# Performance work log

Measured on AMD Instinct MI355X. Metric: run time of the kernel, lower is better.

The kernel has to match this reference:

```python
import jax, jax.numpy as jnp
import numpy as np

B, T, C = 4, 2048, 2048
H, HKV = 16, 4
D = C // H            # 128
G = H // HKV          # 4 query heads per kv head
ROPE_THETA = 10000.0


def _rope_tables(seq_len, head_dim, theta):
    inv = 1.0 / (theta ** (np.arange(0, head_dim, 2, dtype=np.float32) / head_dim))
    t = np.arange(seq_len, dtype=np.float32)
    f = np.outer(t, inv)  # (T, D/2)
    return jnp.asarray(np.cos(f)), jnp.asarray(np.sin(f))


def setup_inputs() -> dict:
    key = jax.random.key(0)
    ks = jax.random.split(key, 5)
    x = jax.random.normal(ks[0], (B, T, C), dtype=jnp.float32)
    W_q = jax.random.normal(ks[1], (H * D, C), dtype=jnp.float32) * 0.02
    W_k = jax.random.normal(ks[2], (HKV * D, C), dtype=jnp.float32) * 0.02
    W_v = jax.random.normal(ks[3], (HKV * D, C), dtype=jnp.float32) * 0.02
    W_o = jax.random.normal(ks[4], (C, C), dtype=jnp.float32) * 0.02
    cos, sin = _rope_tables(T, D, ROPE_THETA)
    return {"x": x, "W_q": W_q, "W_k": W_k, "W_v": W_v, "W_o": W_o,
            "cos": cos, "sin": sin}


def _apply_rope(xh, cos, sin):
    # xh: (B, h, T, D); cos/sin: (T, D/2)
    x0 = xh[..., 0::2]
    x1 = xh[..., 1::2]
    c = cos[None, None, :, :]
    s = sin[None, None, :, :]
    o0 = x0 * c - x1 * s
    o1 = x0 * s + x1 * c
    return jnp.stack([o0, o1], axis=-1).reshape(xh.shape)


def reference(x, W_q, W_k, W_v, W_o, cos, sin):
    b, t, c = x.shape
    q = (x @ W_q.T).reshape(b, t, H, D).transpose(0, 2, 1, 3)      # (B,H,T,D)
    k = (x @ W_k.T).reshape(b, t, HKV, D).transpose(0, 2, 1, 3)    # (B,HKV,T,D)
    v = (x @ W_v.T).reshape(b, t, HKV, D).transpose(0, 2, 1, 3)
    q = _apply_rope(q, cos[:t], sin[:t])
    k = _apply_rope(k, cos[:t], sin[:t])
    # GQA via reshape instead of repeat_interleave (same head ordering:
    # q head index h = kv*G + g).
    qg = q.reshape(b, HKV, G, t, D)
    scores = jnp.einsum('bkgtd,bksd->bkgts', qg, k) / jnp.sqrt(jnp.float32(D))
    causal = jnp.tril(jnp.ones((t, t), dtype=bool))
    scores = jnp.where(causal[None, None, None, :, :], scores, -jnp.inf)
    attn = jax.nn.softmax(scores, axis=-1)
    out = jnp.einsum('bkgts,bksd->bkgtd', attn, v)                 # (B,HKV,G,T,D)
    out = out.reshape(b, H, t, D).transpose(0, 2, 1, 3).reshape(b, t, c)
    return out @ W_o.T
```

## Files before the change

### kernel.cpp

```cpp
#include <hip/hip_runtime.h>
#include <cmath>

typedef __attribute__((ext_vector_type(8))) short bf16x8;
typedef __attribute__((ext_vector_type(4))) float f32x4;
typedef __attribute__((ext_vector_type(16))) float f32x16;
typedef unsigned short u16;

__device__ __forceinline__ u16 f2bf(float f) {
  union { float f; unsigned u; } x; x.f = f;
  return (u16)((x.u + 0x7FFFu + ((x.u >> 16) & 1u)) >> 16);
}

__device__ __forceinline__ unsigned cvtpk(float lo, float hi) {
  unsigned r;
  asm("v_cvt_pk_bf16_f32 %0, %1, %2" : "=v"(r) : "v"(lo), "v"(hi));
  return r;
}

__device__ __forceinline__ void gload_lds16(const void* g, void* l) {
  __builtin_amdgcn_global_load_lds((const __attribute__((address_space(1))) unsigned*)g,
                                   (__attribute__((address_space(3))) unsigned*)l,
                                   16, 0, 0);
}

__global__ __launch_bounds__(256) void cast_all_kernel(const float* __restrict__ x,
                                                       const float* __restrict__ wq,
                                                       const float* __restrict__ wk,
                                                       const float* __restrict__ wv,
                                                       const float* __restrict__ wo,
                                                       u16* __restrict__ out) {
  const long b1 = 16777216, b2 = 20971520, b3 = 22020096, b4 = 23068672, b5 = 27262976;
  long i = (long)blockIdx.x * blockDim.x + threadIdx.x;
  long stride = (long)gridDim.x * blockDim.x;
  for (long j = i * 4; j < b5; j += stride * 4) {
    const float* src; long off;
    if (j < b1)      { src = x;  off = j; }
    else if (j < b2) { src = wq; off = j - b1; }
    else if (j < b3) { src = wk; off = j - b2; }
    else if (j < b4) { src = wv; off = j - b3; }
    else             { src = wo; off = j - b4; }
    float4 v = *(const float4*)(src + off);
    ushort4 o;
    o.x = f2bf(v.x); o.y = f2bf(v.y); o.z = f2bf(v.z); o.w = f2bf(v.w);
    *(ushort4*)(out + j) = o;
  }
}

template <int EPI>
__global__ __launch_bounds__(512, 2) void gemm_bt256(const u16* __restrict__ A,
                                                     const u16* __restrict__ B,
                                                     void* __restrict__ outp,
                                                     int M, int N, int K,
                                                     const float* __restrict__ cosp,
                                                     const float* __restrict__ sinp,
                                                     float scale) {
  __shared__ u16 lds[65536];
  const int tid = threadIdx.x;
  const int lane = tid & 63;
  const int l16 = lane & 15, lhi = lane >> 4;
  const int w = tid >> 6;
  const int wr = w >> 2, wc = w & 3;
  const int m0 = blockIdx.y * 256;
  const int n0 = blockIdx.x * 256;

  f32x4 acc[8][4];
#pragma unroll
  for (int i = 0; i < 8; ++i)
#pragma unroll
    for (int j = 0; j < 4; ++j) acc[i][j] = (f32x4)0.0f;

  const int NT = K >> 6;

  auto stage = [&](int t, int buf) {
    const int k0 = t << 6;
    u16* Ad = lds + buf * 32768;
    u16* Bd = Ad + 16384;
#pragma unroll
    for (int j = 0; j < 4; ++j) {
      int c = tid + j * 512;
      int row = c >> 3;
      int sboff = ((c & 7) * 16) ^ ((row & 7) << 4);
      gload_lds16(A + (size_t)(m0 + row) * K + k0 + (sboff >> 1), Ad + (size_t)c * 8);
    }
#pragma unroll
    for (int j = 0; j < 4; ++j) {
      int c = tid + j * 512;
      int row = c >> 3;
      int sboff = ((c & 7) * 16) ^ ((row & 7) << 4);
      gload_lds16(B + (size_t)(n0 + row) * K + k0 + (sboff >> 1), Bd + (size_t)c * 8);
    }
  };

  stage(0, 0);
  stage(1, 1);

  for (int t = 0; t < NT; ++t) {
    const int cur = t & 1;
    if (t + 1 < NT) { asm volatile("s_waitcnt vmcnt(8)" ::: "memory"); }
    else            { asm volatile("s_waitcnt vmcnt(0)" ::: "memory"); }
    __builtin_amdgcn_s_barrier();
    const char* Ab = (const char*)(lds + cur * 32768);
    const char* Bb = (const char*)(lds + cur * 32768 + 16384);
#pragma unroll
    for (int qm = 0; qm < 2; ++qm)
#pragma unroll
      for (int qn = 0; qn < 2; ++qn) {
        bf16x8 af[4][2], bfr[2][2];
#pragma unroll
        for (int mi = 0; mi < 4; ++mi) {
          int ra = wr * 128 + qm * 64 + mi * 16 + l16;
#pragma unroll
          for (int kk = 0; kk < 2; ++kk)
            af[mi][kk] = *(const bf16x8*)(Ab + ra * 128 + ((kk * 64 + lhi * 16) ^ ((ra & 7) << 4)));
        }
#pragma unroll
        for (int ni = 0; ni < 2; ++ni) {
          int rb = wc * 64 + qn * 32 + ni * 16 + l16;
#pragma unroll
          for (int kk = 0; kk < 2; ++kk)
            bfr[ni][kk] = *(const bf16x8*)(Bb + rb * 128 + ((kk * 64 + lhi * 16) ^ ((rb & 7) << 4)));
        }
        __builtin_amdgcn_s_setprio(1);
#pragma unroll
        for (int kk = 0; kk < 2; ++kk)
#pragma unroll
          for (int mi = 0; mi < 4; ++mi)
#pragma unroll
            for (int ni = 0; ni < 2; ++ni)
              acc[qm * 4 + mi][qn * 2 + ni] = __builtin_amdgcn_mfma_f32_16x16x32_bf16(
                  af[mi][kk], bfr[ni][kk], acc[qm * 4 + mi][qn * 2 + ni], 0, 0, 0);
        __builtin_amdgcn_s_setprio(0);
      }
    asm volatile("s_waitcnt lgkmcnt(0)" ::: "memory");
    __builtin_amdgcn_s_barrier();
    if (t + 2 < NT) stage(t + 2, cur);
  }

  if (EPI == 2) {
    float* o = (float*)outp;
#pragma unroll
    for (int mi8 = 0; mi8 < 8; ++mi8)
#pragma unroll
      for (int r = 0; r < 4; ++r) {
        int row = m0 + wr * 128 + mi8 * 16 + lhi * 4 + r;
#pragma unroll
        for (int nj = 0; nj < 4; ++nj) {
          int col = n0 + wc * 64 + nj * 16 + l16;
          o[(size_t)row * N + col] = acc[mi8][nj][r];
        }
      }
  } else {
    u16* o = (u16*)outp;
    const int nheads = N >> 7;
#pragma unroll
    for (int mi8 = 0; mi8 < 8; ++mi8)
#pragma unroll
      for (int r = 0; r < 4; ++r) {
        int row = m0 + wr * 128 + mi8 * 16 + lhi * 4 + r;
        int b = row >> 11;
        int tt = row & 2047;
#pragma unroll
        for (int nj = 0; nj < 4; ++nj) {
          int col = n0 + wc * 64 + nj * 16 + l16;
          int hh = col >> 7, dd = col & 127;
          float v = acc[mi8][nj][r];
          float p = __shfl_xor(v, 1);
          float c = cosp[tt * 64 + (dd >> 1)];
          float s = sinp[tt * 64 + (dd >> 1)];
          v = (lane & 1) ? fmaf(p, s, v * c) : fmaf(v, c, -p * s);
          v *= scale;
          o[((size_t)(b * nheads + hh) * 2048 + tt) * 128 + dd] = f2bf(v);
        }
      }
  }
}

__global__ __launch_bounds__(256, 2) void gemm_kv(const u16* __restrict__ A,
                                                  const u16* __restrict__ B,
                                                  u16* __restrict__ kp,
                                                  u16* __restrict__ vtp,
                                                  int M, int N, int K,
                                                  const float* __restrict__ cosp,
                                                  const float* __restrict__ sinp) {
  __shared__ u16 lds[32768];
  const int tid = threadIdx.x;
  const int lane = tid & 63;
  const int l16 = lane & 15, lhi = lane >> 4;
  const int w = tid >> 6;
  const int wr = w >> 1, wc = w & 1;
  const int m0 = blockIdx.y * 128;
  const int n0 = blockIdx.x * 128;
  const int wbase = tid - lane;

  f32x4 acc[4][4];
#pragma unroll
  for (int i = 0; i < 4; ++i)
#pragma unroll
    for (int j = 0; j < 4; ++j) acc[i][j] = (f32x4)0.0f;

  const int NT = K >> 6;

  auto stage = [&](int t, int buf) {
    const int k0 = t << 6;
    u16* Ad = lds + buf * 16384;
    u16* Bd = Ad + 8192;
#pragma unroll
    for (int j = 0; j < 4; ++j) {
      int c = tid + j * 256;
      gload_lds16(A + (size_t)(m0 + (c >> 3)) * K + k0 + (c & 7) * 8,
                  Ad + (size_t)(wbase + j * 256) * 8);
    }
#pragma unroll
    for (int j = 0; j < 4; ++j) {
      int c = tid + j * 256;
      gload_lds16(B + (size_t)(n0 + (c >> 3)) * K + k0 + (c & 7) * 8,
                  Bd + (size_t)(wbase + j * 256) * 8);
    }
  };

  stage(0, 0);
  stage(1, 1);

  for (int t = 0; t < NT; ++t) {
    const int cur = t & 1;
    if (t + 1 < NT) { asm volatile("s_waitcnt vmcnt(8)" ::: "memory"); }
    else            { asm volatile("s_waitcnt vmcnt(0)" ::: "memory"); }
    __builtin_amdgcn_s_barrier();
    const u16* As = lds + cur * 16384;
    const u16* Bs = As + 8192;
#pragma unroll
    for (int kk = 0; kk < 64; kk += 32) {
      bf16x8 af[4], bfr[4];
#pragma unroll
      for (int mi = 0; mi < 4; ++mi)
        af[mi] = *(const bf16x8*)&As[(wr * 64 + mi * 16 + l16) * 64 + kk + lhi * 8];
#pragma unroll
      for (int ni = 0; ni < 4; ++ni)
        bfr[ni] = *(const bf16x8*)&Bs[(wc * 64 + ni * 16 + l16) * 64 + kk + lhi * 8];
      __builtin_amdgcn_s_setprio(1);
#pragma unroll
      for (int mi = 0; mi < 4; ++mi)
#pragma unroll
        for (int ni = 0; ni < 4; ++ni)
          acc[mi][ni] = __builtin_amdgcn_mfma_f32_16x16x32_bf16(af[mi], bfr[ni], acc[mi][ni], 0, 0, 0);
      __builtin_amdgcn_s_setprio(0);
    }
    asm volatile("s_waitcnt lgkmcnt(0)" ::: "memory");
    __builtin_amdgcn_s_barrier();
    if (t + 2 < NT) stage(t + 2, cur);
  }

  {
    const int bx = blockIdx.x;
    if (bx < 4) {
#pragma unroll
      for (int mi = 0; mi < 4; ++mi)
#pragma unroll
        for (int r = 0; r < 4; ++r) {
          int row = m0 + wr * 64 + mi * 16 + lhi * 4 + r;
          int b = row >> 11;
          int t = row & 2047;
          size_t base = ((size_t)(b * 4 + bx) * 2048 + t) * 128;
#pragma unroll
          for (int ni = 0; ni < 4; ++ni) {
            int d = wc * 64 + ni * 16 + l16;
            float v = acc[mi][ni][r];
            float p = __shfl_xor(v, 1);
            float c = cosp[t * 64 + (d >> 1)];
            float s = sinp[t * 64 + (d >> 1)];
            v = (lane & 1) ? fmaf(p, s, v * c) : fmaf(v, c, -p * s);
            kp[base + d] = f2bf(v);
          }
        }
    } else {
      const int kvh = bx - 4;
#pragma unroll
      for (int mi = 0; mi < 4; ++mi)
#pragma unroll
        for (int r = 0; r < 4; ++r) {
          int row = m0 + wr * 64 + mi * 16 + lhi * 4 + r;
          int b = row >> 11;
          int t = row & 2047;
          size_t base = ((size_t)(b * 4 + kvh) * 128) * 2048 + t;
#pragma unroll
          for (int ni = 0; ni < 4; ++ni) {
            int d = wc * 64 + ni * 16 + l16;
            vtp[base + (size_t)d * 2048] = f2bf(acc[mi][ni][r]);
          }
        }
    }
  }
}

__global__ __launch_bounds__(512, 2) void attn_kernel(const u16* __restrict__ Q,
                                                      const u16* __restrict__ Kp,
                                                      const u16* __restrict__ Vtp,
                                                      u16* __restrict__ O) {
  __shared__ u16 lds[65536];

  const int tid = threadIdx.x;
  const int lane = tid & 63;
  const int w = tid >> 6;
  const int l5 = lane & 31, hi = lane >> 5;
  const int bid = blockIdx.x;
  const int hb = bid & 63;
  const int pa = bid >> 6;
  const int h = hb >> 2;
  const int b = hb & 3;
  const int kvh = h >> 2;
  const int wbase = tid - lane;

  const u16* Kb = Kp + (size_t)(b * 4 + kvh) * 2048 * 128;
  const u16* Vtb = Vtp + (size_t)(b * 4 + kvh) * 128 * 2048;

  auto stageKV = [&](int kt, int buf) {
    const int t0k = kt * 128;
    u16* Kd = lds + buf * 32768;
    u16* Vd = Kd + 16384;
#pragma unroll
    for (int j = 0; j < 4; ++j) {
      int c = tid + j * 512;
      int row = c >> 4;
      int sboff = ((c & 15) * 16) ^ ((row & 15) << 4);
      gload_lds16(Kb + (size_t)(t0k + row) * 128 + (sboff >> 1),
                  Kd + (size_t)(wbase + j * 512) * 8);
    }
#pragma unroll
    for (int j = 0; j < 4; ++j) {
      int c = tid + j * 512;
      int d = c >> 4;
      int sboff = ((c & 15) * 16) ^ ((d & 7) << 4);
      gload_lds16(Vtb + (size_t)d * 2048 + t0k + (sboff >> 1),
                  Vd + (size_t)(wbase + j * 512) * 8);
    }
  };

  for (int pass = 0; pass < 2; ++pass) {
    const int qt = pass ? (7 - pa) : pa;
    const int q0 = qt * 256;
    const int wrow0 = q0 + w * 32;
    const int qg = wrow0 + l5;

    const u16* Qb = Q + ((size_t)((b * 16 + h) * 2048 + wrow0)) * 128;
    bf16x8 qf[8];
#pragma unroll
    for (int ks = 0; ks < 8; ++ks)
      qf[ks] = *(const bf16x8*)(Qb + (size_t)l5 * 128 + ks * 16 + hi * 8);

    f32x16 oacc[4];
#pragma unroll
    for (int i = 0; i < 4; ++i) oacc[i] = (f32x16)0.0f;
    float m = -3.0e38f, l = 0.0f;

    const int nkt = 2 * qt + 2;
    stageKV(0, 0);

    for (int kt = 0; kt < nkt; ++kt) {
      const int t0 = kt * 128;
      const int cur = kt & 1;
      if (kt + 1 < nkt) {
        stageKV(kt + 1, cur ^ 1);
        asm volatile("s_waitcnt vmcnt(8)" ::: "memory");
      } else {
        asm volatile("s_waitcnt vmcnt(0)" ::: "memory");
      }
      __builtin_amdgcn_s_barrier();

      if (t0 <= wrow0 + 31) {
        const char* vtb = (const char*)(lds + cur * 32768 + 16384);

        float p[2][32];
#pragma unroll
        for (int sub = 0; sub < 2; ++sub) {
          const char* ksb = (const char*)(lds + cur * 32768 + sub * 8192);
#pragma unroll
          for (int kt2 = 0; kt2 < 2; ++kt2) {
            f32x16 sacc = (f32x16)0.0f;
            int row = kt2 * 32 + l5;
            __builtin_amdgcn_s_setprio(1);
#pragma unroll
            for (int ks = 0; ks < 8; ++ks) {
              bf16x8 kf = *(const bf16x8*)(ksb + row * 256 + ((ks * 32 + hi * 16) ^ ((row & 15) << 4)));
              sacc = __builtin_amdgcn_mfma_f32_32x32x16_bf16(kf, qf[ks], sacc, 0, 0, 0);
            }
            __builtin_amdgcn_s_setprio(0);
#pragma unroll
            for (int r = 0; r < 16; ++r) p[sub][kt2 * 16 + r] = sacc[r];
          }
        }

        if (t0 + 127 > wrow0) {
#pragma unroll
          for (int sub = 0; sub < 2; ++sub)
#pragma unroll
            for (int kt2 = 0; kt2 < 2; ++kt2)
#pragma unroll
              for (int r = 0; r < 16; ++r) {
                int kvg = t0 + sub * 64 + kt2 * 32 + (r & 3) + 8 * (r >> 2) + 4 * hi;
                if (kvg > qg) p[sub][kt2 * 16 + r] = -3.0e38f;
              }
        }

        float mx[16];
#pragma unroll
        for (int i = 0; i < 16; ++i)
          mx[i] = fmaxf(fmaxf(p[0][i], p[0][i + 16]), fmaxf(p[1][i], p[1][i + 16]));
#pragma unroll
        for (int i = 0; i < 8; ++i) mx[i] = fmaxf(mx[i], mx[i + 8]);
#pragma unroll
        for (int i = 0; i < 4; ++i) mx[i] = fmaxf(mx[i], mx[i + 4]);
        float rm = fmaxf(fmaxf(mx[0], mx[1]), fmaxf(mx[2], mx[3]));
        rm = fmaxf(rm, __shfl_xor(rm, 32));

        bool defer = __all(rm <= m + 8.0f);
        if (!defer) {
          float mnew = fmaxf(m, rm);
          float sc = exp2f(m - mnew);
          m = mnew;
          l *= sc;
#pragma unroll
          for (int i = 0; i < 4; ++i)
#pragma unroll
            for (int r = 0; r < 16; ++r) oacc[i][r] *= sc;
        }

#pragma unroll
        for (int sub = 0; sub < 2; ++sub)
#pragma unroll
          for (int i = 0; i < 32; ++i) p[sub][i] = exp2f(p[sub][i] - m);
        float sm[16];
#pragma unroll
        for (int i = 0; i < 16; ++i)
          sm[i] = (p[0][i] + p[0][i + 16]) + (p[1][i] + p[1][i + 16]);
#pragma unroll
        for (int i = 0; i < 8; ++i) sm[i] += sm[i + 8];
#pragma unroll
        for (int i = 0; i < 4; ++i) sm[i] += sm[i + 4];
        float s2 = (sm[0] + sm[1]) + (sm[2] + sm[3]);
        s2 += __shfl_xor(s2, 32);
        l += s2;

#pragma unroll
        for (int sub = 0; sub < 2; ++sub) {
          const int vsub = sub * 128;
#pragma unroll
          for (int kt2 = 0; kt2 < 2; ++kt2) {
#pragma unroll
            for (int sl = 0; sl < 2; ++sl) {
              int base = kt2 * 16 + sl * 8;
              unsigned A0 = cvtpk(p[sub][base + 0], p[sub][base + 1]);
              unsigned A1 = cvtpk(p[sub][base + 2], p[sub][base + 3]);
              unsigned A2 = cvtpk(p[sub][base + 4], p[sub][base + 5]);
              unsigned A3 = cvtpk(p[sub][base + 6], p[sub][base + 7]);
              asm volatile("v_permlane32_swap_b32 %0, %1" : "+v"(A0), "+v"(A2));
              asm volatile("v_permlane32_swap_b32 %0, %1" : "+v"(A1), "+v"(A3));
              union { unsigned u[4]; bf16x8 v; } pf;
              pf.u[0] = A0;
              pf.u[1] = A1;
              pf.u[2] = A2;
              pf.u[3] = A3;
              int s = kt2 * 2 + sl;
              __builtin_amdgcn_s_setprio(1);
#pragma unroll
              for (int dt = 0; dt < 4; ++dt) {
                int row = dt * 32 + l5;
                bf16x8 vb = *(const bf16x8*)(vtb + row * 256 + vsub +
                                             ((s * 32 + hi * 16) ^ ((row & 7) << 4)));
                oacc[dt] = __builtin_amdgcn_mfma_f32_32x32x16_bf16(vb, pf.v, oacc[dt], 0, 0, 0);
              }
              __builtin_amdgcn_s_setprio(0);
            }
          }
        }
      }

      asm volatile("s_waitcnt lgkmcnt(0)" ::: "memory");
      __builtin_amdgcn_s_barrier();
    }

    float inv = 1.0f / l;
    __syncthreads();
    for (int half = 0; half < 2; ++half) {
      if ((w >> 2) == half) {
        u16* OSw = lds + (w & 3) * 4352;
#pragma unroll
        for (int dt = 0; dt < 4; ++dt)
#pragma unroll
          for (int r = 0; r < 16; ++r) {
            int d = dt * 32 + (r & 3) + 8 * (r >> 2) + 4 * hi;
            OSw[l5 * 136 + d] = f2bf(oacc[dt][r] * inv);
          }
      }
      __syncthreads();
      u16* Ob = O + ((size_t)(b * 2048 + q0 + half * 128)) * 2048 + h * 128;
#pragma unroll
      for (int j = 0; j < 4; ++j) {
        int c = tid + j * 512;
        int row = c >> 4, col = c & 15;
        *(bf16x8*)(Ob + (size_t)row * 2048 + col * 8) =
            *(const bf16x8*)&lds[(row >> 5) * 4352 + (row & 31) * 136 + col * 8];
      }
      __syncthreads();
    }
  }
}

extern "C" void kernel_launch(void* const* d_in, const int* in_sizes, int n_in,
                              void* d_out, int out_size, void* d_ws, size_t ws_size,
                              hipStream_t stream) {
  (void)in_sizes; (void)n_in; (void)out_size; (void)ws_size;
  const float* x    = (const float*)d_in[0];
  const float* Wq   = (const float*)d_in[1];
  const float* Wk   = (const float*)d_in[2];
  const float* Wv   = (const float*)d_in[3];
  const float* Wo   = (const float*)d_in[4];
  const float* cosp = (const float*)d_in[5];
  const float* sinp = (const float*)d_in[6];

  u16* ws  = (u16*)d_ws;
  u16* xbf = ws;
  u16* Wqb = xbf + 16777216;
  u16* Wkb = Wqb + 4194304;
  u16* Wvb = Wkb + 1048576;
  u16* Wob = Wvb + 1048576;
  u16* Qb  = Wob + 4194304;
  u16* Kb  = Qb + 16777216;
  u16* Vb  = Kb + 4194304;
  u16* AO  = xbf;

  cast_all_kernel<<<2048, 256, 0, stream>>>(x, Wq, Wk, Wv, Wo, ws);

  const float qscale = (float)(1.4426950408889634 / sqrt(128.0));

  gemm_bt256<0><<<dim3(8, 32), 512, 0, stream>>>(xbf, Wqb, Qb, 8192, 2048, 2048, cosp, sinp, qscale);
  gemm_kv<<<dim3(8, 64), 256, 0, stream>>>(xbf, Wkb, Kb, Vb, 8192, 1024, 2048, cosp, sinp);

  attn_kernel<<<256, 512, 0, stream>>>(Qb, Kb, Vb, AO);

  gemm_bt256<2><<<dim3(8, 32), 512, 0, stream>>>(AO, Wob, d_out, 8192, 2048, 2048, nullptr, nullptr, 1.0f);
}
```

Measured before the change: 312.8 us.

## Split GEMM tile staging into half-tiles interleaved with per-quadrant MFMA phases

Restructures the bf16 GEMM main loop so the A and B tiles are loaded in 64-row halves, with each half-load issued inside one of four compute phases rather than as a full stage after the whole tile's compute. The LDS layout is reordered so each quadrant phase reads a contiguous half-buffer. The goal is to spread global-to-LDS traffic across the MFMA work and keep loads in flight continuously. In exchange it adds a barrier per phase and makes the buffer-reuse ordering more intricate, which raises the chance of LDS race bugs.

```diff
diff --git a/kernel.cpp b/kernel.cpp
--- a/kernel.cpp
+++ b/kernel.cpp
@@ -62,6 +62,7 @@
   const int wr = w >> 2, wc = w & 3;
   const int m0 = blockIdx.y * 256;
   const int n0 = blockIdx.x * 256;
+  const int wbase = tid - lane;
 
   f32x4 acc[8][4];
 #pragma unroll
@@ -71,69 +72,83 @@
 
   const int NT = K >> 6;
 
-  auto stage = [&](int t, int buf) {
+  auto stageA = [&](int t, int h) {
     const int k0 = t << 6;
-    u16* Ad = lds + buf * 32768;
-    u16* Bd = Ad + 16384;
-#pragma unroll
-    for (int j = 0; j < 4; ++j) {
+    u16* dst = lds + (t & 1) * 32768 + h * 8192;
+#pragma unroll
+    for (int j = 0; j < 2; ++j) {
       int c = tid + j * 512;
-      int row = c >> 3;
-      int sboff = ((c & 7) * 16) ^ ((row & 7) << 4);
-      gload_lds16(A + (size_t)(m0 + row) * K + k0 + (sboff >> 1), Ad + (size_t)c * 8);
-    }
-#pragma unroll
-    for (int j = 0; j < 4; ++j) {
+      int lr = c >> 3;
+      int arow = ((lr & 64) << 1) + h * 64 + (lr & 63);
+      int sboff = ((c & 7) * 16) ^ ((lr & 7) << 4);
+      gload_lds16(A + (size_t)(m0 + arow) * K + k0 + (sboff >> 1),
+                  dst + (size_t)(wbase + j * 512) * 8);
+    }
+  };
+  auto stageB = [&](int t, int g) {
+    const int k0 = t << 6;
+    u16* dst = lds + (t & 1) * 32768 + 16384 + g * 8192;
+#pragma unroll
+    for (int j = 0; j < 2; ++j) {
       int c = tid + j * 512;
-      int row = c >> 3;
-      int sboff = ((c & 7) * 16) ^ ((row & 7) << 4);
-      gload_lds16(B + (size_t)(n0 + row) * K + k0 + (sboff >> 1), Bd + (size_t)c * 8);
+      int lr = c >> 3;
+      int brow = (lr >> 5) * 64 + g * 32 + (lr & 31);
+      int sboff = ((c & 7) * 16) ^ ((lr & 7) << 4);
+      gload_lds16(B + (size_t)(n0 + brow) * K + k0 + (sboff >> 1),
+                  dst + (size_t)(wbase + j * 512) * 8);
     }
   };
 
-  stage(0, 0);
-  stage(1, 1);
+  stageA(0, 0); stageB(0, 0); stageA(0, 1); stageB(0, 1);
+  stageA(1, 0); stageB(1, 0);
+  asm volatile("s_waitcnt vmcnt(4)" ::: "memory");
+  __builtin_amdgcn_s_barrier();
 
   for (int t = 0; t < NT; ++t) {
     const int cur = t & 1;
-    if (t + 1 < NT) { asm volatile("s_waitcnt vmcnt(8)" ::: "memory"); }
-    else            { asm volatile("s_waitcnt vmcnt(0)" ::: "memory"); }
-    __builtin_amdgcn_s_barrier();
-    const char* Ab = (const char*)(lds + cur * 32768);
-    const char* Bb = (const char*)(lds + cur * 32768 + 16384);
-#pragma unroll
-    for (int qm = 0; qm < 2; ++qm)
-#pragma unroll
-      for (int qn = 0; qn < 2; ++qn) {
-        bf16x8 af[4][2], bfr[2][2];
-#pragma unroll
-        for (int mi = 0; mi < 4; ++mi) {
-          int ra = wr * 128 + qm * 64 + mi * 16 + l16;
-#pragma unroll
-          for (int kk = 0; kk < 2; ++kk)
-            af[mi][kk] = *(const bf16x8*)(Ab + ra * 128 + ((kk * 64 + lhi * 16) ^ ((ra & 7) << 4)));
-        }
-#pragma unroll
-        for (int ni = 0; ni < 2; ++ni) {
-          int rb = wc * 64 + qn * 32 + ni * 16 + l16;
-#pragma unroll
-          for (int kk = 0; kk < 2; ++kk)
-            bfr[ni][kk] = *(const bf16x8*)(Bb + rb * 128 + ((kk * 64 + lhi * 16) ^ ((rb & 7) << 4)));
-        }
-        __builtin_amdgcn_s_setprio(1);
+#pragma unroll
+    for (int ph = 0; ph < 4; ++ph) {
+      const int qm = ph >> 1, qn = ph & 1;
+      const char* Ah = (const char*)(lds + cur * 32768 + qm * 8192);
+      const char* Bh = (const char*)(lds + cur * 32768 + 16384 + qn * 8192);
+      bf16x8 af[4][2], bfr[2][2];
+#pragma unroll
+      for (int mi = 0; mi < 4; ++mi) {
+        int lr = wr * 64 + mi * 16 + l16;
 #pragma unroll
         for (int kk = 0; kk < 2; ++kk)
-#pragma unroll
-          for (int mi = 0; mi < 4; ++mi)
-#pragma unroll
-            for (int ni = 0; ni < 2; ++ni)
-              acc[qm * 4 + mi][qn * 2 + ni] = __builtin_amdgcn_mfma_f32_16x16x32_bf16(
-                  af[mi][kk], bfr[ni][kk], acc[qm * 4 + mi][qn * 2 + ni], 0, 0, 0);
-        __builtin_amdgcn_s_setprio(0);
-      }
-    asm volatile("s_waitcnt lgkmcnt(0)" ::: "memory");
-    __builtin_amdgcn_s_barrier();
-    if (t + 2 < NT) stage(t + 2, cur);
+          af[mi][kk] = *(const bf16x8*)(Ah + lr * 128 + ((kk * 64 + lhi * 16) ^ ((lr & 7) << 4)));
+      }
+#pragma unroll
+      for (int ni = 0; ni < 2; ++ni) {
+        int lr = wc * 32 + ni * 16 + l16;
+#pragma unroll
+        for (int kk = 0; kk < 2; ++kk)
+          bfr[ni][kk] = *(const bf16x8*)(Bh + lr * 128 + ((kk * 64 + lhi * 16) ^ ((lr & 7) << 4)));
+      }
+      if (ph == 0)      { if (t + 1 < NT) stageA(t + 1, 1); }
+      else if (ph == 1) { if (t + 1 < NT) stageB(t + 1, 1); }
+      else if (ph == 2) { if (t + 2 < NT) stageA(t + 2, 0); }
+      else              { if (t + 2 < NT) stageB(t + 2, 0); }
+      __builtin_amdgcn_s_barrier();
+      asm volatile("s_waitcnt lgkmcnt(0)" ::: "memory");
+      __builtin_amdgcn_sched_barrier(0);
+      __builtin_amdgcn_s_setprio(1);
+#pragma unroll
+      for (int kk = 0; kk < 2; ++kk)
+#pragma unroll
+        for (int mi = 0; mi < 4; ++mi)
+#pragma unroll
+          for (int ni = 0; ni < 2; ++ni)
+            acc[qm * 4 + mi][qn * 2 + ni] = __builtin_amdgcn_mfma_f32_16x16x32_bf16(
+                af[mi][kk], bfr[ni][kk], acc[qm * 4 + mi][qn * 2 + ni], 0, 0, 0);
+      __builtin_amdgcn_s_setprio(0);
+      if (ph == 3 && t + 1 < NT) {
+        if (t + 2 < NT) { asm volatile("s_waitcnt vmcnt(4)" ::: "memory"); }
+        else            { asm volatile("s_waitcnt vmcnt(0)" ::: "memory"); }
+      }
+      __builtin_amdgcn_s_barrier();
+    }
   }
 
   if (EPI == 2) {
```

After: 315.8 us. Within noise of the previous version (+0.9%).

## Process paired high and low query tiles in one KV sweep sharing staged K/V

Applied to the files above, without the earlier changes.

Instead of two sequential passes that each stream K/V for a low and a high causal query tile, the kernel now keeps both tiles' accumulators live and runs a single KV loop. Each staged K/V block is reused by both tiles, so the low tile's K/V loads are no longer repeated. The tile body also splits each 128-key block into two 64-key sub-blocks with their own online-softmax update, so fully masked sub-blocks are skipped. The cost is roughly double the accumulator registers, which may cause spills or lower occupancy under the 512x2 launch bounds. Q fragments for the low tile are reloaded from global memory every iteration.

```diff
diff --git a/kernel.cpp b/kernel.cpp
--- a/kernel.cpp
+++ b/kernel.cpp
@@ -310,8 +310,15 @@
   const int kvh = h >> 2;
   const int wbase = tid - lane;
 
+  const int qtH = 7 - pa, qtL = pa;
+  const int q0H = qtH * 256, q0L = qtL * 256;
+  const int wrow0H = q0H + w * 32, wrow0L = q0L + w * 32;
+  const int qgH = wrow0H + l5, qgL = wrow0L + l5;
+
   const u16* Kb = Kp + (size_t)(b * 4 + kvh) * 2048 * 128;
   const u16* Vtb = Vtp + (size_t)(b * 4 + kvh) * 128 * 2048;
+  const u16* QbH = Q + ((size_t)((b * 16 + h) * 2048 + wrow0H)) * 128;
+  const u16* QbL = Q + ((size_t)((b * 16 + h) * 2048 + wrow0L)) * 128;
 
   auto stageKV = [&](int kt, int buf) {
     const int t0k = kt * 128;
@@ -335,76 +342,45 @@
     }
   };
 
-  for (int pass = 0; pass < 2; ++pass) {
-    const int qt = pass ? (7 - pa) : pa;
-    const int q0 = qt * 256;
-    const int wrow0 = q0 + w * 32;
-    const int qg = wrow0 + l5;
-
-    const u16* Qb = Q + ((size_t)((b * 16 + h) * 2048 + wrow0)) * 128;
-    bf16x8 qf[8];
-#pragma unroll
-    for (int ks = 0; ks < 8; ++ks)
-      qf[ks] = *(const bf16x8*)(Qb + (size_t)l5 * 128 + ks * 16 + hi * 8);
-
-    f32x16 oacc[4];
-#pragma unroll
-    for (int i = 0; i < 4; ++i) oacc[i] = (f32x16)0.0f;
-    float m = -3.0e38f, l = 0.0f;
-
-    const int nkt = 2 * qt + 2;
-    stageKV(0, 0);
-
-    for (int kt = 0; kt < nkt; ++kt) {
-      const int t0 = kt * 128;
-      const int cur = kt & 1;
-      if (kt + 1 < nkt) {
-        stageKV(kt + 1, cur ^ 1);
-        asm volatile("s_waitcnt vmcnt(8)" ::: "memory");
-      } else {
-        asm volatile("s_waitcnt vmcnt(0)" ::: "memory");
-      }
-      __builtin_amdgcn_s_barrier();
-
-      if (t0 <= wrow0 + 31) {
+  auto tile_body = [&](const bf16x8 (&qf)[8], f32x16 (&oacc)[4], float& m, float& l,
+                       int wrow0, int qg, int t0, int cur) {
+#pragma unroll
+    for (int sub = 0; sub < 2; ++sub) {
+      const int t0s = t0 + sub * 64;
+      if (t0s <= wrow0 + 31) {
+        const char* ksb = (const char*)(lds + cur * 32768 + sub * 8192);
         const char* vtb = (const char*)(lds + cur * 32768 + 16384);
-
-        float p[2][32];
-#pragma unroll
-        for (int sub = 0; sub < 2; ++sub) {
-          const char* ksb = (const char*)(lds + cur * 32768 + sub * 8192);
-#pragma unroll
-          for (int kt2 = 0; kt2 < 2; ++kt2) {
-            f32x16 sacc = (f32x16)0.0f;
-            int row = kt2 * 32 + l5;
-            __builtin_amdgcn_s_setprio(1);
-#pragma unroll
-            for (int ks = 0; ks < 8; ++ks) {
-              bf16x8 kf = *(const bf16x8*)(ksb + row * 256 + ((ks * 32 + hi * 16) ^ ((row & 15) << 4)));
-              sacc = __builtin_amdgcn_mfma_f32_32x32x16_bf16(kf, qf[ks], sacc, 0, 0, 0);
+        const int vsub = sub * 128;
+
+        float p[32];
+#pragma unroll
+        for (int kt2 = 0; kt2 < 2; ++kt2) {
+          f32x16 sacc = (f32x16)0.0f;
+          int row = kt2 * 32 + l5;
+          __builtin_amdgcn_s_setprio(1);
+#pragma unroll
+          for (int ks = 0; ks < 8; ++ks) {
+            bf16x8 kf = *(const bf16x8*)(ksb + row * 256 + ((ks * 32 + hi * 16) ^ ((row & 15) << 4)));
+            sacc = __builtin_amdgcn_mfma_f32_32x32x16_bf16(kf, qf[ks], sacc, 0, 0, 0);
+          }
+          __builtin_amdgcn_s_setprio(0);
+#pragma unroll
+          for (int r = 0; r < 16; ++r) p[kt2 * 16 + r] = sacc[r];
+        }
+
+        if (t0s + 63 > wrow0) {
+#pragma unroll
+          for (int kt2 = 0; kt2 < 2; ++kt2)
+#pragma unroll
+            for (int r = 0; r < 16; ++r) {
+              int kvg = t0s + kt2 * 32 + (r & 3) + 8 * (r >> 2) + 4 * hi;
+              if (kvg > qg) p[kt2 * 16 + r] = -3.0e38f;
             }
-            __builtin_amdgcn_s_setprio(0);
-#pragma unroll
-            for (int r = 0; r < 16; ++r) p[sub][kt2 * 16 + r] = sacc[r];
-          }
-        }
-
-        if (t0 + 127 > wrow0) {
-#pragma unroll
-          for (int sub = 0; sub < 2; ++sub)
-#pragma unroll
-            for (int kt2 = 0; kt2 < 2; ++kt2)
-#pragma unroll
-              for (int r = 0; r < 16; ++r) {
-                int kvg = t0 + sub * 64 + kt2 * 32 + (r & 3) + 8 * (r >> 2) + 4 * hi;
-                if (kvg > qg) p[sub][kt2 * 16 + r] = -3.0e38f;
-              }
         }
 
         float mx[16];
 #pragma unroll
-        for (int i = 0; i < 16; ++i)
-          mx[i] = fmaxf(fmaxf(p[0][i], p[0][i + 16]), fmaxf(p[1][i], p[1][i + 16]));
+        for (int i = 0; i < 16; ++i) mx[i] = fmaxf(p[i], p[i + 16]);
 #pragma unroll
         for (int i = 0; i < 8; ++i) mx[i] = fmaxf(mx[i], mx[i + 8]);
 #pragma unroll
@@ -425,13 +401,10 @@
         }
 
 #pragma unroll
-        for (int sub = 0; sub < 2; ++sub)
-#pragma unroll
-          for (int i = 0; i < 32; ++i) p[sub][i] = exp2f(p[sub][i] - m);
+        for (int i = 0; i < 32; ++i) p[i] = exp2f(p[i] - m);
         float sm[16];
 #pragma unroll
-        for (int i = 0; i < 16; ++i)
-          sm[i] = (p[0][i] + p[0][i + 16]) + (p[1][i] + p[1][i + 16]);
+        for (int i = 0; i < 16; ++i) sm[i] = p[i] + p[i + 16];
 #pragma unroll
         for (int i = 0; i < 8; ++i) sm[i] += sm[i + 8];
 #pragma unroll
@@ -441,45 +414,83 @@
         l += s2;
 
 #pragma unroll
-        for (int sub = 0; sub < 2; ++sub) {
-          const int vsub = sub * 128;
-#pragma unroll
-          for (int kt2 = 0; kt2 < 2; ++kt2) {
-#pragma unroll
-            for (int sl = 0; sl < 2; ++sl) {
-              int base = kt2 * 16 + sl * 8;
-              unsigned A0 = cvtpk(p[sub][base + 0], p[sub][base + 1]);
-              unsigned A1 = cvtpk(p[sub][base + 2], p[sub][base + 3]);
-              unsigned A2 = cvtpk(p[sub][base + 4], p[sub][base + 5]);
-              unsigned A3 = cvtpk(p[sub][base + 6], p[sub][base + 7]);
-              asm volatile("v_permlane32_swap_b32 %0, %1" : "+v"(A0), "+v"(A2));
-              asm volatile("v_permlane32_swap_b32 %0, %1" : "+v"(A1), "+v"(A3));
-              union { unsigned u[4]; bf16x8 v; } pf;
-              pf.u[0] = A0;
-              pf.u[1] = A1;
-              pf.u[2] = A2;
-              pf.u[3] = A3;
-              int s = kt2 * 2 + sl;
-              __builtin_amdgcn_s_setprio(1);
-#pragma unroll
-              for (int dt = 0; dt < 4; ++dt) {
-                int row = dt * 32 + l5;
-                bf16x8 vb = *(const bf16x8*)(vtb + row * 256 + vsub +
-                                             ((s * 32 + hi * 16) ^ ((row & 7) << 4)));
-                oacc[dt] = __builtin_amdgcn_mfma_f32_32x32x16_bf16(vb, pf.v, oacc[dt], 0, 0, 0);
-              }
-              __builtin_amdgcn_s_setprio(0);
+        for (int kt2 = 0; kt2 < 2; ++kt2) {
+#pragma unroll
+          for (int sl = 0; sl < 2; ++sl) {
+            int base = kt2 * 16 + sl * 8;
+            unsigned A0 = cvtpk(p[base + 0], p[base + 1]);
+            unsigned A1 = cvtpk(p[base + 2], p[base + 3]);
+            unsigned A2 = cvtpk(p[base + 4], p[base + 5]);
+            unsigned A3 = cvtpk(p[base + 6], p[base + 7]);
+            asm volatile("v_permlane32_swap_b32 %0, %1" : "+v"(A0), "+v"(A2));
+            asm volatile("v_permlane32_swap_b32 %0, %1" : "+v"(A1), "+v"(A3));
+            union { unsigned u[4]; bf16x8 v; } pf;
+            pf.u[0] = A0;
+            pf.u[1] = A1;
+            pf.u[2] = A2;
+            pf.u[3] = A3;
+            int s = kt2 * 2 + sl;
+            __builtin_amdgcn_s_setprio(1);
+#pragma unroll
+            for (int dt = 0; dt < 4; ++dt) {
+              int row = dt * 32 + l5;
+              bf16x8 vb = *(const bf16x8*)(vtb + row * 256 + vsub +
+                                           ((s * 32 + hi * 16) ^ ((row & 7) << 4)));
+              oacc[dt] = __builtin_amdgcn_mfma_f32_32x32x16_bf16(vb, pf.v, oacc[dt], 0, 0, 0);
             }
+            __builtin_amdgcn_s_setprio(0);
           }
         }
       }
-
-      asm volatile("s_waitcnt lgkmcnt(0)" ::: "memory");
-      __builtin_amdgcn_s_barrier();
-    }
-
-    float inv = 1.0f / l;
-    __syncthreads();
+    }
+  };
+
+  bf16x8 qfH[8];
+#pragma unroll
+  for (int ks = 0; ks < 8; ++ks)
+    qfH[ks] = *(const bf16x8*)(QbH + (size_t)l5 * 128 + ks * 16 + hi * 8);
+
+  f32x16 oaccH[4], oaccL[4];
+#pragma unroll
+  for (int i = 0; i < 4; ++i) { oaccH[i] = (f32x16)0.0f; oaccL[i] = (f32x16)0.0f; }
+  float mH = -3.0e38f, lH = 0.0f, mL = -3.0e38f, lL = 0.0f;
+
+  const int nkt = 2 * qtH + 2;
+  stageKV(0, 0);
+
+  for (int kt = 0; kt < nkt; ++kt) {
+    const int t0 = kt * 128;
+    const int cur = kt & 1;
+    const bool Lact = (t0 <= wrow0L + 31);
+
+    bf16x8 qfL[8];
+    if (Lact) {
+#pragma unroll
+      for (int ks = 0; ks < 8; ++ks)
+        qfL[ks] = *(const bf16x8*)(QbL + (size_t)l5 * 128 + ks * 16 + hi * 8);
+      __builtin_amdgcn_sched_barrier(0);
+    }
+    if (kt + 1 < nkt) stageKV(kt + 1, cur ^ 1);
+
+    if (Lact)               { asm volatile("s_waitcnt vmcnt(16)" ::: "memory"); }
+    else if (kt + 1 < nkt)  { asm volatile("s_waitcnt vmcnt(8)" ::: "memory"); }
+    else                    { asm volatile("s_waitcnt vmcnt(0)" ::: "memory"); }
+    __builtin_amdgcn_s_barrier();
+
+    if (t0 <= wrow0H + 31)
+      tile_body(qfH, oaccH, mH, lH, wrow0H, qgH, t0, cur);
+    if (Lact)
+      tile_body(qfL, oaccL, mL, lL, wrow0L, qgL, t0, cur);
+
+    asm volatile("s_waitcnt lgkmcnt(0)" ::: "memory");
+    __builtin_amdgcn_s_barrier();
+  }
+
+  __syncthreads();
+#pragma unroll
+  for (int tile = 0; tile < 2; ++tile) {
+    const int q0 = tile ? q0L : q0H;
+    const float inv = 1.0f / (tile ? lL : lH);
     for (int half = 0; half < 2; ++half) {
       if ((w >> 2) == half) {
         u16* OSw = lds + (w & 3) * 4352;
@@ -488,7 +499,7 @@
 #pragma unroll
           for (int r = 0; r < 16; ++r) {
             int d = dt * 32 + (r & 3) + 8 * (r >> 2) + 4 * hi;
-            OSw[l5 * 136 + d] = f2bf(oacc[dt][r] * inv);
+            OSw[l5 * 136 + d] = f2bf((tile ? oaccL[dt][r] : oaccH[dt][r]) * inv);
           }
       }
       __syncthreads();
```

Measured after the change: 404.3 us. 1.29x slower.
